# Performance work log

Measured on AMD Instinct MI355X. Metric: run time of the kernel, lower is better.

The kernel has to match this reference:

```python
import jax, jax.numpy as jnp
import numpy as np

M_POS = 0.5
M_NEG_SIM = 0.1
LAM_NEG = 1.0


def setup_inputs() -> dict:
    key = jax.random.key(0)
    N, d, G = 8192, 1024, 64
    codebook = jax.random.normal(key, (N, d), dtype=jnp.float32)
    base = (jnp.arange(N) // G) * G  # contiguous groups of size G (vq_to_range)
    starts = base.astype(jnp.int32)
    ends = (base + G - 1).astype(jnp.int32)
    return {"codebook": codebook, "starts": starts, "ends": ends, "max_i": N - 1}


def reference(codebook, starts, ends, max_i):
    N, d = codebook.shape
    M = min(N, int(max_i) + 1)  # rows processed by the python loop

    # cosine similarity rows [0:M] vs all N
    zn = codebook / jnp.linalg.norm(codebook, axis=-1, keepdims=True)
    cos = jnp.einsum('md,nd->mn', zn[:M], zn)  # (M, N)

    # pairwise Euclidean distances rows [0:M] vs all N via ||a-b||^2 = |a|^2+|b|^2-2ab
    sq = jnp.sum(codebook * codebook, axis=-1)  # (N,)
    dot = jnp.einsum('md,nd->mn', codebook[:M], codebook)  # (M, N)
    d2 = jnp.maximum(sq[:M, None] + sq[None, :] - 2.0 * dot, 0.0)

    j = jnp.arange(N)[None, :]
    i = jnp.arange(M)[:, None]
    in_range = (j >= starts[:M, None]) & (j <= ends[:M, None])
    pos_mask = in_range & (j != i)
    # original: group_mask[i]=False then neg = ~group_mask, so i is in negatives
    neg_mask = (~in_range) | (j == i)

    pos_cnt = jnp.sum(pos_mask, axis=-1)
    neg_cnt = jnp.sum(neg_mask, axis=-1)

    # safe sqrt: only evaluate on positive-mask entries
    D = jnp.sqrt(jnp.where(pos_mask, d2, 1.0))
    pos_term = jnp.square(jax.nn.relu(D - M_POS)) * pos_mask
    pos_pull = jnp.sum(pos_term, axis=-1) / jnp.maximum(pos_cnt, 1)

    neg_cos = jnp.clip(cos, -1.0, 1.0)
    neg_term = jnp.square(jax.nn.relu(jnp.abs(neg_cos) - M_NEG_SIM)) * neg_mask
    ortho = jnp.sum(neg_term, axis=-1) / jnp.maximum(neg_cnt, 1)

    valid = (pos_cnt > 0) & (neg_cnt > 0)
    per_row = jnp.where(valid, pos_pull + LAM_NEG * ortho, 0.0)
    cnt = jnp.sum(valid)
    total = jnp.sum(per_row)
    return jnp.where(cnt > 0, total / jnp.maximum(cnt, 1).astype(total.dtype), jnp.zeros((), total.dtype))
```

## Files before the change

kernel.cpp:

```cpp
#include <hip/hip_runtime.h>
#include <hip/hip_bf16.h>
#include <stdint.h>

#define M_POS 0.5f
#define M_NEG 0.1f
#define LAM_NEG 1.0f

typedef __attribute__((ext_vector_type(4))) float floatx4;
typedef __attribute__((ext_vector_type(8))) int   intx8;
typedef __attribute__((ext_vector_type(4))) int   int32x4;

union Frag8 { intx8 v; int4 q[2]; };

__global__ __launch_bounds__(256) void prep_kernel(
    const float* __restrict__ cb, unsigned char* __restrict__ cb_q,
    float* __restrict__ sq, float* __restrict__ inv_norm,
    unsigned* __restrict__ zero_base, int zero_len,
    int N, int d)
{
    const int gi = blockIdx.x * 256 + threadIdx.x;
    if (gi < zero_len) zero_base[gi] = 0u;

    const int t = threadIdx.x;
    const int w = t >> 6, l = t & 63;
    const int row = blockIdx.x * 4 + w;
    if (row >= N) return;
    const float* src = cb + (size_t)row * d;
    unsigned char* dst = cb_q + (size_t)row * d;

    float s = 0.f;
    for (int c = l * 16; c < d; c += 1024) {
        float4 v0 = *(const float4*)(src + c);
        float4 v1 = *(const float4*)(src + c + 4);
        float4 v2 = *(const float4*)(src + c + 8);
        float4 v3 = *(const float4*)(src + c + 12);
        s += v0.x*v0.x + v0.y*v0.y + v0.z*v0.z + v0.w*v0.w
           + v1.x*v1.x + v1.y*v1.y + v1.z*v1.z + v1.w*v1.w
           + v2.x*v2.x + v2.y*v2.y + v2.z*v2.z + v2.w*v2.w
           + v3.x*v3.x + v3.y*v3.y + v3.z*v3.z + v3.w*v3.w;
        int p0 = __builtin_amdgcn_cvt_pk_fp8_f32(v0.x, v0.y, 0, false);
        p0     = __builtin_amdgcn_cvt_pk_fp8_f32(v0.z, v0.w, p0, true);
        int p1 = __builtin_amdgcn_cvt_pk_fp8_f32(v1.x, v1.y, 0, false);
        p1     = __builtin_amdgcn_cvt_pk_fp8_f32(v1.z, v1.w, p1, true);
        int p2 = __builtin_amdgcn_cvt_pk_fp8_f32(v2.x, v2.y, 0, false);
        p2     = __builtin_amdgcn_cvt_pk_fp8_f32(v2.z, v2.w, p2, true);
        int p3 = __builtin_amdgcn_cvt_pk_fp8_f32(v3.x, v3.y, 0, false);
        p3     = __builtin_amdgcn_cvt_pk_fp8_f32(v3.z, v3.w, p3, true);
        int32x4 pk; pk.x = p0; pk.y = p1; pk.z = p2; pk.w = p3;
        *(int32x4*)(dst + c) = pk;
    }
    for (int o = 32; o > 0; o >>= 1) s += __shfl_down(s, o, 64);
    if (l == 0) { sq[row] = s; inv_norm[row] = rsqrtf(s); }
}

__global__ __launch_bounds__(512, 1) void gram_loss_kernel(
    const unsigned char* __restrict__ A,
    const float* __restrict__ sq, const float* __restrict__ inv_norm,
    const int* __restrict__ starts, const int* __restrict__ ends,
    const int* __restrict__ max_ip,
    float* __restrict__ pos_acc, float* __restrict__ neg_acc,
    unsigned* __restrict__ counter, float* __restrict__ out,
    int N, int d)
{
    const int M = min(N, max_ip[0] + 1);

    int vt = blockIdx.x;
    const int nB = gridDim.x;
    if ((nB & 7) == 0) {
        const int per = nB >> 3;
        vt = (blockIdx.x & 7) * per + (blockIdx.x >> 3);
    }

    int bx = (int)((sqrtf(8.f * (float)vt + 1.f) - 1.f) * 0.5f);
    while ((bx + 1) * (bx + 2) / 2 <= vt) bx++;
    while (bx * (bx + 1) / 2 > vt) bx--;
    const int by = vt - bx * (bx + 1) / 2;

    const int rowBase = by * 256;
    const int colBase = bx * 256;
    const bool isDiag = (by == bx);

    __shared__ alignas(16) unsigned char ldsA[2][256 * 128];
    __shared__ alignas(16) unsigned char ldsB[2][256 * 128];

    const int tid  = threadIdx.x;
    const int wave = tid >> 6;
    const int lane = tid & 63;
    const int wr = (wave >> 2) * 128;
    const int wc = (wave & 3) * 64;

    floatx4 acc[8][4];
#pragma unroll
    for (int a = 0; a < 8; ++a)
#pragma unroll
        for (int b = 0; b < 4; ++b) acc[a][b] = (floatx4){0.f, 0.f, 0.f, 0.f};

    const int sRow8 = tid >> 3;
    const int sChk  = tid & 7;
    const int srcOffC = ((sChk ^ (sRow8 & 7)) * 16);
    const int kTiles = d / 128;

    const int rl = lane & 15;
    const int g  = lane >> 4;
    const int rx = rl & 7;
    const int c0 = (((2 * g)     ^ rx) * 16);
    const int c1 = (((2 * g + 1) ^ rx) * 16);

#define STAGE(SLOT, KT)                                                         \
    { const int k0_ = (KT) * 128;                                               \
      _Pragma("unroll")                                                         \
      for (int h = 0; h < 4; ++h) {                                             \
        const int r_ = h * 64 + sRow8;                                          \
        const unsigned char* ga_ = A + (size_t)(rowBase + r_) * d + k0_ + srcOffC; \
        const unsigned char* gb_ = A + (size_t)(colBase + r_) * d + k0_ + srcOffC; \
        __builtin_amdgcn_global_load_lds(                                       \
            (const __attribute__((address_space(1))) void*)ga_,                 \
            (__attribute__((address_space(3))) void*)(ldsA[SLOT] + r_ * 128 + sChk * 16), 16, 0, 0); \
        __builtin_amdgcn_global_load_lds(                                       \
            (const __attribute__((address_space(1))) void*)gb_,                 \
            (__attribute__((address_space(3))) void*)(ldsB[SLOT] + r_ * 128 + sChk * 16), 16, 0, 0); \
      } }

#define WAITV(NN)  asm volatile("s_waitcnt vmcnt(" #NN ")" ::: "memory")

    if (kTiles == 8) {
        STAGE(0, 0)
        __builtin_amdgcn_sched_barrier(0);
        STAGE(1, 1)
        __builtin_amdgcn_sched_barrier(0);
#pragma unroll
        for (int kt = 0; kt < 8; ++kt) {
            const int cur = kt & 1;
            if (kt < 7) { WAITV(8); } else { WAITV(0); }
            __builtin_amdgcn_s_barrier();

            Frag8 bfr[4];
#pragma unroll
            for (int ct = 0; ct < 4; ++ct) {
                const unsigned char* pb = ldsB[cur] + (wc + ct * 16 + rl) * 128;
                bfr[ct].q[0] = *(const int4*)(pb + c0);
                bfr[ct].q[1] = *(const int4*)(pb + c1);
            }
#pragma unroll
            for (int ph = 0; ph < 4; ++ph) {
                Frag8 af0, af1;
                const unsigned char* pa0 = ldsA[cur] + (wr + (2 * ph) * 16 + rl) * 128;
                const unsigned char* pa1 = ldsA[cur] + (wr + (2 * ph + 1) * 16 + rl) * 128;
                af0.q[0] = *(const int4*)(pa0 + c0);
                af0.q[1] = *(const int4*)(pa0 + c1);
                af1.q[0] = *(const int4*)(pa1 + c0);
                af1.q[1] = *(const int4*)(pa1 + c1);
                __builtin_amdgcn_s_setprio(1);
#pragma unroll
                for (int ct = 0; ct < 4; ++ct)
                    acc[2 * ph][ct] = __builtin_amdgcn_mfma_scale_f32_16x16x128_f8f6f4(
                        af0.v, bfr[ct].v, acc[2 * ph][ct], 0, 0, 0, 127, 0, 127);
#pragma unroll
                for (int ct = 0; ct < 4; ++ct)
                    acc[2 * ph + 1][ct] = __builtin_amdgcn_mfma_scale_f32_16x16x128_f8f6f4(
                        af1.v, bfr[ct].v, acc[2 * ph + 1][ct], 0, 0, 0, 127, 0, 127);
                __builtin_amdgcn_s_setprio(0);
                __builtin_amdgcn_sched_barrier(0);
            }

            __builtin_amdgcn_s_barrier();
            if (kt + 2 < 8) {
                STAGE(cur, kt + 2)
                __builtin_amdgcn_sched_barrier(0);
            }
        }
    } else {
        for (int kt = 0; kt < kTiles; ++kt) {
            STAGE(0, kt)
            WAITV(0);
            __builtin_amdgcn_s_barrier();
            Frag8 bfr[4];
#pragma unroll
            for (int ct = 0; ct < 4; ++ct) {
                const unsigned char* pb = ldsB[0] + (wc + ct * 16 + rl) * 128;
                bfr[ct].q[0] = *(const int4*)(pb + c0);
                bfr[ct].q[1] = *(const int4*)(pb + c1);
            }
#pragma unroll
            for (int rt = 0; rt < 8; ++rt) {
                Frag8 af;
                const unsigned char* pa = ldsA[0] + (wr + rt * 16 + rl) * 128;
                af.q[0] = *(const int4*)(pa + c0);
                af.q[1] = *(const int4*)(pa + c1);
#pragma unroll
                for (int ct = 0; ct < 4; ++ct)
                    acc[rt][ct] = __builtin_amdgcn_mfma_scale_f32_16x16x128_f8f6f4(
                        af.v, bfr[ct].v, acc[rt][ct], 0, 0, 0, 127, 0, 127);
            }
            __syncthreads();
        }
    }
#undef STAGE
#undef WAITV

    const int q  = lane >> 4;
    const int jlo = colBase + wc;
    const int ilo = rowBase + wr;

    int   jn[4];
    float jinv[4];
    bool  jvalid[4];
#pragma unroll
    for (int ct = 0; ct < 4; ++ct) {
        const int j = jlo + ct * 16 + rl;
        jn[ct]  = j;
        jinv[ct] = inv_norm[j];
        jvalid[ct] = (j < M);
    }

    bool posLane = false;
    {
        const int ri0 = ilo + lane;
        const int ri1 = ilo + 64 + lane;
        if (ri0 < M) posLane |= (ends[ri0] >= jlo) && (starts[ri0] <= jlo + 63);
        if (ri1 < M) posLane |= (ends[ri1] >= jlo) && (starts[ri1] <= jlo + 63);
        if (!isDiag) {
            const int cj = jlo + lane;
            if (cj < M) posLane |= (ends[cj] >= ilo) && (starts[cj] <= ilo + 127);
        }
    }
    const bool fullPath = (__ballot(posLane) != 0ULL);

    float posc[4] = {0.f, 0.f, 0.f, 0.f};
    float negc[4] = {0.f, 0.f, 0.f, 0.f};

    if (fullPath) {
        int   jns[4], jne[4];
        float jsq[4];
#pragma unroll
        for (int ct = 0; ct < 4; ++ct) {
            jsq[ct] = sq[jn[ct]];
            jns[ct] = jvalid[ct] ? starts[jn[ct]] : 0;
            jne[ct] = jvalid[ct] ? ends[jn[ct]]   : -1;
        }
#pragma unroll
        for (int rt = 0; rt < 8; ++rt) {
            const int ibase = ilo + rt * 16 + q * 4;
#pragma unroll
            for (int reg = 0; reg < 4; ++reg) {
                const int i = ibase + reg;
                const bool rowValid = (i < M);
                const int ns = rowValid ? starts[i] : 0;
                const int ne = rowValid ? ends[i]   : -1;
                const float iinv = inv_norm[i];
                const float isq  = sq[i];
                float posp = 0.f, negp = 0.f;
#pragma unroll
                for (int ct = 0; ct < 4; ++ct) {
                    const float dot = acc[rt][ct][reg];
                    const int j = jn[ct];
                    float cosv = dot * iinv * jinv[ct];
                    cosv = fminf(fmaxf(cosv, -1.f), 1.f);
                    float tn = fmaxf(fabsf(cosv) - M_NEG, 0.f);
                    const float nterm = tn * tn;
                    const float d2 = fmaxf(isq + jsq[ct] - 2.f * dot, 0.f);
                    float tp = fmaxf(sqrtf(d2) - M_POS, 0.f);
                    const float pterm = tp * tp;
                    const bool dg = (j == i);
                    if (rowValid) {
                        const bool in_r = (j >= ns) && (j <= ne);
                        if (in_r && !dg) posp += pterm;
                        if (!in_r || dg) negp += nterm;
                    }
                    if (!isDiag && jvalid[ct]) {
                        const bool in_c = (i >= jns[ct]) && (i <= jne[ct]);
                        if (in_c && !dg) posc[ct] += pterm;
                        if (!in_c || dg) negc[ct] += nterm;
                    }
                }
#pragma unroll
                for (int m = 1; m < 16; m <<= 1) {
                    posp += __shfl_xor(posp, m, 64);
                    negp += __shfl_xor(negp, m, 64);
                }
                if (rowValid && rl == 0) {
                    atomicAdd(&pos_acc[i], posp);
                    atomicAdd(&neg_acc[i], negp);
                }
            }
        }
        if (!isDiag) {
#pragma unroll
            for (int ct = 0; ct < 4; ++ct) {
                posc[ct] += __shfl_xor(posc[ct], 16, 64);
                posc[ct] += __shfl_xor(posc[ct], 32, 64);
                negc[ct] += __shfl_xor(negc[ct], 16, 64);
                negc[ct] += __shfl_xor(negc[ct], 32, 64);
            }
            if (q == 0) {
#pragma unroll
                for (int ct = 0; ct < 4; ++ct) {
                    if (jvalid[ct]) {
                        atomicAdd(&pos_acc[jn[ct]], posc[ct]);
                        atomicAdd(&neg_acc[jn[ct]], negc[ct]);
                    }
                }
            }
        }
    } else {
#pragma unroll
        for (int rt = 0; rt < 8; ++rt) {
            const int ibase = ilo + rt * 16 + q * 4;
#pragma unroll
            for (int reg = 0; reg < 4; ++reg) {
                const int i = ibase + reg;
                const float iinv = inv_norm[i];
                float negp = 0.f;
#pragma unroll
                for (int ct = 0; ct < 4; ++ct) {
                    const float dot = acc[rt][ct][reg];
                    float cosv = dot * iinv * jinv[ct];
                    cosv = fminf(fmaxf(cosv, -1.f), 1.f);
                    float tn = fmaxf(fabsf(cosv) - M_NEG, 0.f);
                    const float nterm = tn * tn;
                    negp += nterm;
                    negc[ct] += nterm;
                }
#pragma unroll
                for (int m = 1; m < 16; m <<= 1)
                    negp += __shfl_xor(negp, m, 64);
                if ((i < M) && rl == 0)
                    atomicAdd(&neg_acc[i], negp);
            }
        }
        if (!isDiag) {
#pragma unroll
            for (int ct = 0; ct < 4; ++ct) {
                negc[ct] += __shfl_xor(negc[ct], 16, 64);
                negc[ct] += __shfl_xor(negc[ct], 32, 64);
            }
            if (q == 0) {
#pragma unroll
                for (int ct = 0; ct < 4; ++ct)
                    if (jvalid[ct])
                        atomicAdd(&neg_acc[jn[ct]], negc[ct]);
            }
        }
    }

    struct FinSm { int amLast; float ts[8]; int cs[8]; };
    FinSm* fs = (FinSm*)&ldsA[0][0];
    __syncthreads();
    if (tid == 0) {
        __threadfence();
        unsigned old = atomicAdd(counter, 1u);
        fs->amLast = (old == (unsigned)(gridDim.x - 1)) ? 1 : 0;
    }
    __syncthreads();
    if (fs->amLast) {
        __threadfence();
        float total = 0.f;
        int cnt = 0;
        for (int i = tid; i < M; i += 512) {
            const float pa = __hip_atomic_load(&pos_acc[i], __ATOMIC_RELAXED, __HIP_MEMORY_SCOPE_AGENT);
            const float na = __hip_atomic_load(&neg_acc[i], __ATOMIC_RELAXED, __HIP_MEMORY_SCOPE_AGENT);
            const int ns = starts[i], ne = ends[i];
            const int lo = max(ns, 0), hi = min(ne, N - 1);
            const int inr = max(hi - lo + 1, 0);
            const bool dg = (i >= ns) && (i <= ne);
            const int pos_cnt = inr - (dg ? 1 : 0);
            const int neg_cnt = N - inr + (dg ? 1 : 0);
            if (pos_cnt > 0 && neg_cnt > 0) {
                total += pa / (float)max(pos_cnt, 1)
                       + LAM_NEG * na / (float)max(neg_cnt, 1);
                cnt++;
            }
        }
        for (int o = 32; o > 0; o >>= 1) {
            total += __shfl_down(total, o, 64);
            cnt   += __shfl_down(cnt, o, 64);
        }
        if (lane == 0) { fs->ts[wave] = total; fs->cs[wave] = cnt; }
        __syncthreads();
        if (tid == 0) {
            float T = 0.f; int C = 0;
            for (int wv = 0; wv < 8; ++wv) { T += fs->ts[wv]; C += fs->cs[wv]; }
            out[0] = (C > 0) ? T / (float)C : 0.f;
        }
    }
}

extern "C" void kernel_launch(void* const* d_in, const int* in_sizes, int n_in,
                              void* d_out, int out_size, void* d_ws, size_t ws_size,
                              hipStream_t stream) {
    const float* cb     = (const float*)d_in[0];
    const int*   starts = (const int*)d_in[1];
    const int*   ends   = (const int*)d_in[2];
    const int*   max_ip = (const int*)d_in[3];
    float* out = (float*)d_out;

    const int N = in_sizes[1];
    const int d = in_sizes[0] / N;

    char* ws = (char*)d_ws;
    unsigned char* cb_q = (unsigned char*)ws;
    size_t off = ((size_t)N * d + 255) & ~(size_t)255;
    float* sq       = (float*)(ws + off); off += (size_t)N * 4;
    float* inv_norm = (float*)(ws + off); off += (size_t)N * 4;
    float* pos_acc  = (float*)(ws + off); off += (size_t)N * 4;
    float* neg_acc  = (float*)(ws + off); off += (size_t)N * 4;
    unsigned* counter = (unsigned*)(ws + off); off += 256;

    prep_kernel<<<(N + 3) / 4, 256, 0, stream>>>(cb, cb_q, sq, inv_norm,
                                                 (unsigned*)pos_acc, 2 * N + 1, N, d);

    const int nb = N / 256;
    const int nBlocks = nb * (nb + 1) / 2;
    gram_loss_kernel<<<nBlocks, 512, 0, stream>>>(cb_q, sq, inv_norm, starts, ends,
                                                  max_ip, pos_acc, neg_acc, counter,
                                                  out, N, d);
}
```

Measured before the change: 202.4 us.

## Generalize double-buffered gram loop and narrow prep kernel loads

```diff
diff --git a/kernel.cpp b/kernel.cpp
--- a/kernel.cpp
+++ b/kernel.cpp
@@ -8,7 +8,6 @@
 
 typedef __attribute__((ext_vector_type(4))) float floatx4;
 typedef __attribute__((ext_vector_type(8))) int   intx8;
-typedef __attribute__((ext_vector_type(4))) int   int32x4;
 
 union Frag8 { intx8 v; int4 q[2]; };
 
@@ -29,25 +28,12 @@
     unsigned char* dst = cb_q + (size_t)row * d;
 
     float s = 0.f;
-    for (int c = l * 16; c < d; c += 1024) {
-        float4 v0 = *(const float4*)(src + c);
-        float4 v1 = *(const float4*)(src + c + 4);
-        float4 v2 = *(const float4*)(src + c + 8);
-        float4 v3 = *(const float4*)(src + c + 12);
-        s += v0.x*v0.x + v0.y*v0.y + v0.z*v0.z + v0.w*v0.w
-           + v1.x*v1.x + v1.y*v1.y + v1.z*v1.z + v1.w*v1.w
-           + v2.x*v2.x + v2.y*v2.y + v2.z*v2.z + v2.w*v2.w
-           + v3.x*v3.x + v3.y*v3.y + v3.z*v3.z + v3.w*v3.w;
-        int p0 = __builtin_amdgcn_cvt_pk_fp8_f32(v0.x, v0.y, 0, false);
-        p0     = __builtin_amdgcn_cvt_pk_fp8_f32(v0.z, v0.w, p0, true);
-        int p1 = __builtin_amdgcn_cvt_pk_fp8_f32(v1.x, v1.y, 0, false);
-        p1     = __builtin_amdgcn_cvt_pk_fp8_f32(v1.z, v1.w, p1, true);
-        int p2 = __builtin_amdgcn_cvt_pk_fp8_f32(v2.x, v2.y, 0, false);
-        p2     = __builtin_amdgcn_cvt_pk_fp8_f32(v2.z, v2.w, p2, true);
-        int p3 = __builtin_amdgcn_cvt_pk_fp8_f32(v3.x, v3.y, 0, false);
-        p3     = __builtin_amdgcn_cvt_pk_fp8_f32(v3.z, v3.w, p3, true);
-        int32x4 pk; pk.x = p0; pk.y = p1; pk.z = p2; pk.w = p3;
-        *(int32x4*)(dst + c) = pk;
+    for (int c = l * 4; c < d; c += 256) {
+        float4 v = *(const float4*)(src + c);
+        s += v.x * v.x + v.y * v.y + v.z * v.z + v.w * v.w;
+        int pk = __builtin_amdgcn_cvt_pk_fp8_f32(v.x, v.y, 0, false);
+        pk     = __builtin_amdgcn_cvt_pk_fp8_f32(v.z, v.w, pk, true);
+        *(int*)(dst + c) = pk;
     }
     for (int o = 32; o > 0; o >>= 1) s += __shfl_down(s, o, 64);
     if (l == 0) { sq[row] = s; inv_norm[row] = rsqrtf(s); }
@@ -112,10 +98,10 @@
       for (int h = 0; h < 4; ++h) {                                             \
         const int r_ = h * 64 + sRow8;                                          \
         const unsigned char* ga_ = A + (size_t)(rowBase + r_) * d + k0_ + srcOffC; \
-        const unsigned char* gb_ = A + (size_t)(colBase + r_) * d + k0_ + srcOffC; \
         __builtin_amdgcn_global_load_lds(                                       \
             (const __attribute__((address_space(1))) void*)ga_,                 \
             (__attribute__((address_space(3))) void*)(ldsA[SLOT] + r_ * 128 + sChk * 16), 16, 0, 0); \
+        const unsigned char* gb_ = A + (size_t)(colBase + r_) * d + k0_ + srcOffC; \
         __builtin_amdgcn_global_load_lds(                                       \
             (const __attribute__((address_space(1))) void*)gb_,                 \
             (__attribute__((address_space(3))) void*)(ldsB[SLOT] + r_ * 128 + sChk * 16), 16, 0, 0); \
@@ -123,15 +109,15 @@
 
 #define WAITV(NN)  asm volatile("s_waitcnt vmcnt(" #NN ")" ::: "memory")
 
-    if (kTiles == 8) {
+    {
         STAGE(0, 0)
         __builtin_amdgcn_sched_barrier(0);
         STAGE(1, 1)
         __builtin_amdgcn_sched_barrier(0);
-#pragma unroll
-        for (int kt = 0; kt < 8; ++kt) {
+
+        for (int kt = 0; kt < kTiles; ++kt) {
             const int cur = kt & 1;
-            if (kt < 7) { WAITV(8); } else { WAITV(0); }
+            if (kt < kTiles - 1) { WAITV(8); } else { WAITV(0); }
             __builtin_amdgcn_s_barrier();
 
             Frag8 bfr[4];
@@ -141,50 +127,11 @@
                 bfr[ct].q[0] = *(const int4*)(pb + c0);
                 bfr[ct].q[1] = *(const int4*)(pb + c1);
             }
-#pragma unroll
-            for (int ph = 0; ph < 4; ++ph) {
-                Frag8 af0, af1;
-                const unsigned char* pa0 = ldsA[cur] + (wr + (2 * ph) * 16 + rl) * 128;
-                const unsigned char* pa1 = ldsA[cur] + (wr + (2 * ph + 1) * 16 + rl) * 128;
-                af0.q[0] = *(const int4*)(pa0 + c0);
-                af0.q[1] = *(const int4*)(pa0 + c1);
-                af1.q[0] = *(const int4*)(pa1 + c0);
-                af1.q[1] = *(const int4*)(pa1 + c1);
-                __builtin_amdgcn_s_setprio(1);
-#pragma unroll
-                for (int ct = 0; ct < 4; ++ct)
-                    acc[2 * ph][ct] = __builtin_amdgcn_mfma_scale_f32_16x16x128_f8f6f4(
-                        af0.v, bfr[ct].v, acc[2 * ph][ct], 0, 0, 0, 127, 0, 127);
-#pragma unroll
-                for (int ct = 0; ct < 4; ++ct)
-                    acc[2 * ph + 1][ct] = __builtin_amdgcn_mfma_scale_f32_16x16x128_f8f6f4(
-                        af1.v, bfr[ct].v, acc[2 * ph + 1][ct], 0, 0, 0, 127, 0, 127);
-                __builtin_amdgcn_s_setprio(0);
-                __builtin_amdgcn_sched_barrier(0);
-            }
-
-            __builtin_amdgcn_s_barrier();
-            if (kt + 2 < 8) {
-                STAGE(cur, kt + 2)
-                __builtin_amdgcn_sched_barrier(0);
-            }
-        }
-    } else {
-        for (int kt = 0; kt < kTiles; ++kt) {
-            STAGE(0, kt)
-            WAITV(0);
-            __builtin_amdgcn_s_barrier();
-            Frag8 bfr[4];
-#pragma unroll
-            for (int ct = 0; ct < 4; ++ct) {
-                const unsigned char* pb = ldsB[0] + (wc + ct * 16 + rl) * 128;
-                bfr[ct].q[0] = *(const int4*)(pb + c0);
-                bfr[ct].q[1] = *(const int4*)(pb + c1);
-            }
+            __builtin_amdgcn_s_setprio(1);
 #pragma unroll
             for (int rt = 0; rt < 8; ++rt) {
                 Frag8 af;
-                const unsigned char* pa = ldsA[0] + (wr + rt * 16 + rl) * 128;
+                const unsigned char* pa = ldsA[cur] + (wr + rt * 16 + rl) * 128;
                 af.q[0] = *(const int4*)(pa + c0);
                 af.q[1] = *(const int4*)(pa + c1);
 #pragma unroll
@@ -192,7 +139,14 @@
                     acc[rt][ct] = __builtin_amdgcn_mfma_scale_f32_16x16x128_f8f6f4(
                         af.v, bfr[ct].v, acc[rt][ct], 0, 0, 0, 127, 0, 127);
             }
-            __syncthreads();
+            __builtin_amdgcn_s_setprio(0);
+            __builtin_amdgcn_sched_barrier(0);
+
+            __builtin_amdgcn_s_barrier();
+            if (kt + 2 < kTiles) {
+                STAGE(cur, kt + 2)
+                __builtin_amdgcn_sched_barrier(0);
+            }
         }
     }
 #undef STAGE
```

Measured after the change: 216.7 us. 1.07x slower.
